# Kernel tuning notes

Hardware: AMD Instinct MI355X
Metric: run time of the kernel (lower is better)

The kernel has to match this reference:

```python
import jax, jax.numpy as jnp
import numpy as np

B, T, N, I = 64, 12, 307, 3   # batch, timesteps, nodes, input features
R, D = 64, 10                 # rnn_units, embed_dim


def setup_inputs() -> dict:
    key = jax.random.key(0)
    ks = iter(jax.random.split(key, 64))
    def p(*shape):
        return jax.random.normal(next(ks), shape, jnp.float32) * 0.1
    return dict(
        x=jax.random.normal(next(ks), (B, T, N, I), jnp.float32),
        node_emb1=p(N, D), node_emb2=p(N, D),
        # x_embedding MLP: 1 -> 16 -> 2 -> D
        xe_w1=p(16, 1), xe_b1=p(16), xe_w2=p(2, 16), xe_b2=p(2), xe_w3=p(D, 2), xe_b3=p(D),
        # fc1 MLP: I -> 16 -> 2 -> D
        fc1_w1=p(16, I), fc1_b1=p(16), fc1_w2=p(2, 16), fc1_b2=p(2), fc1_w3=p(D, 2), fc1_b3=p(D),
        # fc2 MLP: R -> 16 -> 2 -> D
        fc2_w1=p(16, R), fc2_b1=p(16), fc2_w2=p(2, 16), fc2_b2=p(2), fc2_w3=p(D, 2), fc2_b3=p(D),
        # GRU1 (input D -> hidden R), gates ordered r,z,n as in torch
        gru1_wih=p(3 * R, D), gru1_whh=p(3 * R, R), gru1_bih=p(3 * R), gru1_bhh=p(3 * R),
        # GRU2 (input R -> hidden R)
        gru2_wih=p(3 * R, R), gru2_whh=p(3 * R, R), gru2_bih=p(3 * R), gru2_bhh=p(3 * R),
        weights_pool=p(D, R, R), bias_pool=p(D, R),
        # 1x1 conv == linear over channels: [R, 2R]
        diff_w=p(R, 2 * R), diff_b=p(R),
    )


def _mlp(x, w1, b1, w2, b2, w3, b3):
    h = jax.nn.sigmoid(x @ w1.T + b1)
    h = jax.nn.sigmoid(h @ w2.T + b2)
    return h @ w3.T + b3


def _gru(xs, h0, wih, whh, bih, bhh):
    # xs: [T, B', Din]; torch GRU gate order: r, z, n
    xw = xs @ wih.T + bih  # precompute input projections [T, B', 3R]
    def step(h, xw_t):
        hw = h @ whh.T + bhh
        xr, xz, xn = jnp.split(xw_t, 3, -1)
        hr, hz, hn = jnp.split(hw, 3, -1)
        r = jax.nn.sigmoid(xr + hr)
        z = jax.nn.sigmoid(xz + hz)
        n = jnp.tanh(xn + r * hn)
        h = (1.0 - z) * n + z * h
        return h, h
    _, out = jax.lax.scan(step, h0, xw)
    return out  # [T, B', R]


def reference(x, node_emb1, node_emb2,
              xe_w1, xe_b1, xe_w2, xe_b2, xe_w3, xe_b3,
              fc1_w1, fc1_b1, fc1_w2, fc1_b2, fc1_w3, fc1_b3,
              fc2_w1, fc2_b1, fc2_w2, fc2_b2, fc2_w3, fc2_b3,
              gru1_wih, gru1_whh, gru1_bih, gru1_bhh,
              gru2_wih, gru2_whh, gru2_bih, gru2_bhh,
              weights_pool, bias_pool, diff_w, diff_b):
    # --- feature-level dynamic dependency ---
    node_embed = _mlp(x[..., None], xe_w1, xe_b1, xe_w2, xe_b2, xe_w3, xe_b3)  # [B,T,N,I,D]
    supports_node2 = jax.nn.relu(jnp.einsum('btnjd,btnid->btnji', node_embed, node_embed))  # [B,T,N,I,I]
    # x1 = eye(I) @ x == x (identity support kept implicit)
    x2 = jnp.einsum('btnji,btni->btnj', supports_node2, x)
    input_for_fc1 = x + x2
    g1_in = _mlp(input_for_fc1, fc1_w1, fc1_b1, fc1_w2, fc1_b2, fc1_w3, fc1_b3)  # [B,T,N,D]
    g1_in = jnp.transpose(g1_in, (1, 0, 2, 3)).reshape(T, B * N, D)
    h0 = jnp.zeros((B * N, R), jnp.float32)
    out1 = _gru(g1_in, h0, gru1_wih, gru1_whh, gru1_bih, gru1_bhh).reshape(T, B, N, R)
    # --- node-level dynamic dependency ---
    filt = _mlp(out1, fc2_w1, fc2_b1, fc2_w2, fc2_b2, fc2_w3, fc2_b3)  # [T,B,N,D]
    nodevec = jnp.tanh(node_emb1 * filt)  # broadcast [N,D] over [T,B,N,D]
    supports2 = jax.nn.relu(jnp.einsum('tbnd,tbmd->tbnm', nodevec, nodevec))  # [T,B,N,N]
    # x_g1 = eye(N) @ out1 == out1
    x_g = out1 + jnp.einsum('tbnm,tbmc->tbnc', supports2, out1)
    weights = jnp.einsum('nd,dcr->ncr', node_emb2, weights_pool)  # [N,R,R]
    bias = node_emb2 @ bias_pool                                   # [N,R]
    diff1 = jnp.einsum('tbnc,ncr->tbnr', x_g, weights) + bias      # [T,B,N,R]
    # --- 1x1 conv over channels + GRU2 (dropout in eval mode: identity) ---
    cat = jnp.concatenate([out1, diff1], axis=-1)                  # [T,B,N,2R]
    g2_in = jnp.einsum('tbnc,rc->tbnr', cat, diff_w) + diff_b      # [T,B,N,R]
    out2 = _gru(g2_in.reshape(T, B * N, R), h0, gru2_wih, gru2_whh, gru2_bih, gru2_bhh)
    return jnp.transpose(out2.reshape(T, B, N, R), (1, 0, 2, 3))   # [B,T,N,R]
```

## Files before the change

kernel.cpp:

```cpp
#include <hip/hip_runtime.h>
#include <hip/hip_fp16.h>
#include <math.h>

#define B_ 64
#define T_ 12
#define N_ 307
#define I_ 3
#define R_ 64
#define D_ 10
#define M_ (B_*N_)
#define TM_ (T_*M_)

typedef _Float16 f16x8 __attribute__((ext_vector_type(8)));
typedef float f32x4 __attribute__((ext_vector_type(4)));

__device__ __forceinline__ float sigm(float x){ return 1.f/(1.f+__expf(-x)); }

__device__ __forceinline__ unsigned pkh(float a, float b){
  unsigned r;
  asm("v_cvt_pkrtz_f16_f32 %0, %1, %2" : "=v"(r) : "v"(a), "v"(b));
  return r;
}

__global__ __launch_bounds__(256) void k_stageA(
    const float* __restrict__ x,
    const float* __restrict__ xw1, const float* __restrict__ xb1,
    const float* __restrict__ xw2, const float* __restrict__ xb2,
    const float* __restrict__ xw3, const float* __restrict__ xb3,
    const float* __restrict__ fw1, const float* __restrict__ fb1,
    const float* __restrict__ fw2, const float* __restrict__ fb2,
    const float* __restrict__ fw3, const float* __restrict__ fb3,
    float* __restrict__ g1)
{
  int idx = blockIdx.x*256 + threadIdx.x;
  int t = idx / M_;
  int m = idx - t*M_;
  int b = m / N_;
  int n = m - b*N_;
  const float* xp = x + (((size_t)b*T_ + t)*N_ + n)*I_;
  float xv[3] = {xp[0], xp[1], xp[2]};
  float e[3][10];
  #pragma unroll
  for (int i=0;i<3;++i){
    float h1[16];
    #pragma unroll
    for (int u=0;u<16;++u) h1[u] = sigm(xv[i]*xw1[u] + xb1[u]);
    float h2[2];
    #pragma unroll
    for (int v=0;v<2;++v){
      float a = xb2[v];
      #pragma unroll
      for (int u=0;u<16;++u) a += h1[u]*xw2[v*16+u];
      h2[v] = sigm(a);
    }
    #pragma unroll
    for (int d=0;d<10;++d) e[i][d] = xb3[d] + h2[0]*xw3[d*2] + h2[1]*xw3[d*2+1];
  }
  float in1[3];
  #pragma unroll
  for (int j=0;j<3;++j){
    float acc = 0.f;
    #pragma unroll
    for (int i=0;i<3;++i){
      float s = 0.f;
      #pragma unroll
      for (int d=0;d<10;++d) s += e[j][d]*e[i][d];
      s = fmaxf(s, 0.f);
      acc += s*xv[i];
    }
    in1[j] = xv[j] + acc;
  }
  float h1[16];
  #pragma unroll
  for (int u=0;u<16;++u)
    h1[u] = sigm(fb1[u] + in1[0]*fw1[u*3] + in1[1]*fw1[u*3+1] + in1[2]*fw1[u*3+2]);
  float h2[2];
  #pragma unroll
  for (int v=0;v<2;++v){
    float a = fb2[v];
    #pragma unroll
    for (int u=0;u<16;++u) a += h1[u]*fw2[v*16+u];
    h2[v] = sigm(a);
  }
  float* gp = g1 + (size_t)idx*10;
  #pragma unroll
  for (int d=0;d<10;++d) gp[d] = fb3[d] + h2[0]*fw3[d*2] + h2[1]*fw3[d*2+1];
}

__global__ __launch_bounds__(256) void k_wn(
    const float* __restrict__ emb2, const float* __restrict__ wpool,
    const float* __restrict__ bpool, float* __restrict__ Wn, float* __restrict__ bn)
{
  int n = blockIdx.x; int tid = threadIdx.x;
  __shared__ float e_s[10];
  if (tid < 10) e_s[tid] = emb2[n*10 + tid];
  __syncthreads();
  #pragma unroll
  for (int e=0;e<16;++e){
    int i = e*256 + tid;
    float a = 0.f;
    #pragma unroll
    for (int d=0;d<10;++d) a += e_s[d]*wpool[(size_t)d*4096 + i];
    Wn[(size_t)n*4096 + i] = a;
  }
  if (tid < 64){
    float a = 0.f;
    #pragma unroll
    for (int d=0;d<10;++d) a += e_s[d]*bpool[d*64 + tid];
    bn[n*64 + tid] = a;
  }
}

__global__ __launch_bounds__(256) void k_wf(
    const float* __restrict__ Wn, const float* __restrict__ bn,
    const float* __restrict__ dw, const float* __restrict__ db,
    float* __restrict__ Wf, float* __restrict__ bf)
{
  int n = blockIdx.x; int tid = threadIdx.x;
  __shared__ float WnS[64*68];
  __shared__ float dwBT[64*68];
  __shared__ float bn_s[64];
  for (int idx = tid; idx < 4096; idx += 256) {
    int c = idx >> 6, r = idx & 63;
    WnS[c*68 + r] = Wn[(size_t)n*4096 + idx];
  }
  for (int idx = tid; idx < 4096; idx += 256) {
    int u = idx >> 6, r = idx & 63;
    dwBT[r*68 + u] = dw[u*128 + 64 + r];
  }
  if (tid < 64) bn_s[tid] = bn[n*64 + tid];
  __syncthreads();
  int u = tid & 63, cg = tid >> 6;
  #pragma unroll
  for (int j = 0; j < 16; ++j) {
    int c = cg*16 + j;
    float acc = 0.f;
    #pragma unroll 8
    for (int r = 0; r < 64; ++r) acc += WnS[c*68 + r] * dwBT[r*68 + u];
    Wf[(size_t)n*4096 + u*64 + c] = acc;
  }
  if (tid < 64) {
    float acc = db[tid];
    #pragma unroll 8
    for (int r = 0; r < 64; ++r) acc += bn_s[r] * dwBT[r*68 + tid];
    bf[n*64 + tid] = acc;
  }
}

__global__ __launch_bounds__(256) void k_wpackM(
    const float* __restrict__ wih2, const float* __restrict__ whh2,
    const float* __restrict__ wih1, const float* __restrict__ whh1,
    unsigned* __restrict__ Wh2, unsigned* __restrict__ Wx2,
    unsigned* __restrict__ Wh1, unsigned* __restrict__ Wx1)
{
  int i = blockIdx.x*256 + threadIdx.x;
  if (i < 192*32) {
    int wr = i >> 5, p = i & 31;
    Wh2[i] = pkh(whh2[wr*64 + 2*p], whh2[wr*64 + 2*p + 1]);
    Wx2[i] = pkh(wih2[wr*64 + 2*p], wih2[wr*64 + 2*p + 1]);
    Wh1[i] = pkh(whh1[wr*64 + 2*p], whh1[wr*64 + 2*p + 1]);
  }
  int j = i - 192*32;
  if (j >= 0 && j < 192*16) {
    int wr = j >> 4, p = j & 15;
    Wx1[j] = (p < 5) ? pkh(wih1[wr*10 + 2*p], wih1[wr*10 + 2*p + 1]) : 0u;
  }
}

template<int DIN, bool WFIN>
__global__ __launch_bounds__(256, 3) void k_gruM(
    const float* __restrict__ xseq,
    const unsigned* __restrict__ Whf,
    const unsigned* __restrict__ Wxf,
    const float* __restrict__ bih, const float* __restrict__ bhh,
    float* __restrict__ o_out)
{
  constexpr int XPR = (DIN == 64) ? 32 : 16;
  constexpr int XKS = XPR / 16;
  constexpr int XST = XPR + 4;
  __shared__ __align__(16) unsigned Ah_s[16*36];
  __shared__ __align__(16) unsigned Ax_s[16*XST];
  const int tid = threadIdx.x;
  const int lane = tid & 63, w = tid >> 6;
  const int fr = lane & 15, fq = lane >> 4;
  const int row0 = blockIdx.x * 16;
  const int u = w*16 + fr;

  f16x8 bh_r[2], bh_z[2], bh_n[2];
  #pragma unroll
  for (int ks = 0; ks < 2; ++ks) {
    bh_r[ks] = *(const f16x8*)&Whf[(size_t)u*32        + ks*16 + fq*4];
    bh_z[ks] = *(const f16x8*)&Whf[(size_t)(64+u)*32   + ks*16 + fq*4];
    bh_n[ks] = *(const f16x8*)&Whf[(size_t)(128+u)*32  + ks*16 + fq*4];
  }
  f16x8 bx_r[XKS], bx_z[XKS], bx_n[XKS];
  #pragma unroll
  for (int ks = 0; ks < XKS; ++ks) {
    bx_r[ks] = *(const f16x8*)&Wxf[(size_t)u*XPR       + ks*16 + fq*4];
    bx_z[ks] = *(const f16x8*)&Wxf[(size_t)(64+u)*XPR  + ks*16 + fq*4];
    bx_n[ks] = *(const f16x8*)&Wxf[(size_t)(128+u)*XPR + ks*16 + fq*4];
  }

  const float brc = bih[u]     + bhh[u];
  const float bzc = bih[64+u]  + bhh[64+u];
  const float bxn = bih[128+u];
  const float bhn = bhh[128+u];

  for (int i = tid; i < 16*36;  i += 256) Ah_s[i] = 0u;
  for (int i = tid; i < 16*XST; i += 256) Ax_s[i] = 0u;
  __syncthreads();

  size_t obase[4];
  #pragma unroll
  for (int reg = 0; reg < 4; ++reg) {
    int g = row0 + fq*4 + reg;
    if (WFIN) { int bb = g / N_, nn = g - bb*N_; obase[reg] = (((size_t)bb*T_)*N_ + nn)*64 + u; }
    else      { obase[reg] = (size_t)g*64 + u; }
  }
  const size_t tstep = WFIN ? (size_t)N_*64 : (size_t)M_*64;
  float hreg[4] = {0.f, 0.f, 0.f, 0.f};

  for (int t = 0; t < T_; ++t) {
    if (DIN == 64) {
      #pragma unroll
      for (int it = 0; it < 2; ++it) {
        int idx = tid + it*256;
        int row = idx >> 5, p = idx & 31;
        const float2 v = *(const float2*)&xseq[((size_t)t*M_ + row0 + row)*64 + 2*p];
        Ax_s[row*XST + p] = pkh(v.x, v.y);
      }
    } else {
      if (tid < 80) {
        int row = tid / 5, p = tid - (tid/5)*5;
        const float2 v = *(const float2*)&xseq[((size_t)t*M_ + row0 + row)*10 + 2*p];
        Ax_s[row*XST + p] = pkh(v.x, v.y);
      }
    }
    __syncthreads();

    f32x4 ar  = {0.f,0.f,0.f,0.f}, az  = {0.f,0.f,0.f,0.f};
    f32x4 anh = {0.f,0.f,0.f,0.f}, anx = {0.f,0.f,0.f,0.f};
    #pragma unroll
    for (int ks = 0; ks < 2; ++ks) {
      f16x8 ah = *(const f16x8*)&Ah_s[fr*36 + ks*16 + fq*4];
      ar  = __builtin_amdgcn_mfma_f32_16x16x32_f16(ah, bh_r[ks], ar,  0,0,0);
      az  = __builtin_amdgcn_mfma_f32_16x16x32_f16(ah, bh_z[ks], az,  0,0,0);
      anh = __builtin_amdgcn_mfma_f32_16x16x32_f16(ah, bh_n[ks], anh, 0,0,0);
    }
    #pragma unroll
    for (int ks = 0; ks < XKS; ++ks) {
      f16x8 ax = *(const f16x8*)&Ax_s[fr*XST + ks*16 + fq*4];
      ar  = __builtin_amdgcn_mfma_f32_16x16x32_f16(ax, bx_r[ks], ar,  0,0,0);
      az  = __builtin_amdgcn_mfma_f32_16x16x32_f16(ax, bx_z[ks], az,  0,0,0);
      anx = __builtin_amdgcn_mfma_f32_16x16x32_f16(ax, bx_n[ks], anx, 0,0,0);
    }

    float o_new[4];
    #pragma unroll
    for (int reg = 0; reg < 4; ++reg) {
      float rg = sigm(ar[reg] + brc);
      float zg = sigm(az[reg] + bzc);
      float ng = tanhf(anx[reg] + bxn + rg*(anh[reg] + bhn));
      o_new[reg] = (1.f - zg)*ng + zg*hreg[reg];
      hreg[reg] = o_new[reg];
    }
    #pragma unroll
    for (int reg = 0; reg < 4; ++reg)
      o_out[obase[reg] + (size_t)t*tstep] = o_new[reg];

    unsigned pk[4];
    #pragma unroll
    for (int reg = 0; reg < 4; ++reg) {
      float pr = __shfl_xor(o_new[reg], 1);
      pk[reg] = pkh(o_new[reg], pr);
    }
    __syncthreads();
    if ((fr & 1) == 0) {
      #pragma unroll
      for (int reg = 0; reg < 4; ++reg)
        Ah_s[(fq*4 + reg)*36 + w*8 + (fr >> 1)] = pk[reg];
    }
  }
}

__global__ __launch_bounds__(256) void k_stageC(
    const float* __restrict__ out1, const float* __restrict__ emb1,
    const float* __restrict__ w1, const float* __restrict__ b1,
    const float* __restrict__ w2, const float* __restrict__ b2,
    const float* __restrict__ w3, const float* __restrict__ b3,
    float* __restrict__ ndv)
{
  int idx = blockIdx.x*256 + threadIdx.x;
  int m = idx % M_;
  int n = m % N_;
  float rv[64];
  const float4* r4 = (const float4*)(out1 + (size_t)idx*64);
  #pragma unroll
  for (int q=0;q<16;++q){ float4 v=r4[q]; rv[q*4]=v.x; rv[q*4+1]=v.y; rv[q*4+2]=v.z; rv[q*4+3]=v.w; }
  float h1[16];
  for (int u=0;u<16;++u){
    float a = b1[u];
    const float* wr = w1 + u*64;
    #pragma unroll
    for (int c=0;c<64;++c) a += rv[c]*wr[c];
    h1[u] = sigm(a);
  }
  float h2[2];
  #pragma unroll
  for (int v=0;v<2;++v){
    float a = b2[v];
    #pragma unroll
    for (int u=0;u<16;++u) a += h1[u]*w2[v*16+u];
    h2[v] = sigm(a);
  }
  #pragma unroll
  for (int d=0;d<10;++d){
    float f = b3[d] + h2[0]*w3[d*2] + h2[1]*w3[d*2+1];
    ndv[(size_t)idx*10 + d] = tanhf(emb1[n*10+d]*f);
  }
}

__global__ __launch_bounds__(256, 3) void k_stageDM(
    const float* __restrict__ ndv, const float* __restrict__ out1, float* __restrict__ xg)
{
  const int tb = blockIdx.x;
  const int tid = threadIdx.x;
  const int lane = tid & 63, wid = tid >> 6;
  const int fr = lane & 15, fq = lane >> 4;

  __shared__ __align__(16) unsigned Vp_s[320*20];
  __shared__ __align__(16) unsigned P_s[64*36];
  __shared__ __align__(16) unsigned O_s[2][64*36];

  for (int i = tid; i < 320*20; i += 256) {
    int nn = i / 20, p = i - (i/20)*20;
    float a = 0.f, b = 0.f;
    if (nn < N_ && p < 5) {
      const float2 v = *(const float2*)&ndv[((size_t)tb*N_ + nn)*10 + 2*p];
      a = v.x; b = v.y;
    }
    Vp_s[i] = pkh(a, b);
  }

  const float* ob = out1 + (size_t)tb*N_*64;

  for (int it = tid; it < 512; it += 256) {
    int p = it & 31, cg = it >> 5;
    int m0 = 2*p;
    float4 a = make_float4(0.f,0.f,0.f,0.f), b = a;
    if (m0     < N_) a = *(const float4*)&ob[(size_t)m0*64 + cg*4];
    if (m0 + 1 < N_) b = *(const float4*)&ob[(size_t)(m0+1)*64 + cg*4];
    int c0 = cg*4;
    O_s[0][(c0+0)*36 + p] = pkh(a.x, b.x);
    O_s[0][(c0+1)*36 + p] = pkh(a.y, b.y);
    O_s[0][(c0+2)*36 + p] = pkh(a.z, b.z);
    O_s[0][(c0+3)*36 + p] = pkh(a.w, b.w);
  }
  __syncthreads();

  f32x4 acc[5][4];
  #pragma unroll
  for (int a = 0; a < 5; ++a)
    #pragma unroll
    for (int c = 0; c < 4; ++c)
      acc[a][c] = (f32x4){0.f, 0.f, 0.f, 0.f};

  for (int k = 0; k < 5; ++k) {
    const int cur = k & 1;
    const int mc = k*64;
    if (k < 4) {
      int mcn = mc + 64;
      for (int it = tid; it < 512; it += 256) {
        int p = it & 31, cg = it >> 5;
        int m0 = mcn + 2*p;
        float4 a = make_float4(0.f,0.f,0.f,0.f), b = a;
        if (m0     < N_) a = *(const float4*)&ob[(size_t)m0*64 + cg*4];
        if (m0 + 1 < N_) b = *(const float4*)&ob[(size_t)(m0+1)*64 + cg*4];
        int c0 = cg*4;
        O_s[cur^1][(c0+0)*36 + p] = pkh(a.x, b.x);
        O_s[cur^1][(c0+1)*36 + p] = pkh(a.y, b.y);
        O_s[cur^1][(c0+2)*36 + p] = pkh(a.z, b.z);
        O_s[cur^1][(c0+3)*36 + p] = pkh(a.w, b.w);
      }
    }
    f16x8 va[4];
    #pragma unroll
    for (int mt = 0; mt < 4; ++mt)
      va[mt] = *(const f16x8*)&Vp_s[(mc + mt*16 + fr)*20 + fq*4];
    f16x8 bo[2][4];
    #pragma unroll
    for (int ks = 0; ks < 2; ++ks)
      #pragma unroll
      for (int ct = 0; ct < 4; ++ct)
        bo[ks][ct] = *(const f16x8*)&O_s[cur][(ct*16 + fr)*36 + ks*16 + fq*4];

    #pragma unroll
    for (int j = 0; j < 5; ++j) {
      int nt = wid + 4*j;
      f16x8 vb = *(const f16x8*)&Vp_s[(nt*16 + fr)*20 + fq*4];
      #pragma unroll
      for (int mt = 0; mt < 4; ++mt) {
        f32x4 s = (f32x4){0.f,0.f,0.f,0.f};
        s = __builtin_amdgcn_mfma_f32_16x16x32_f16(va[mt], vb, s, 0, 0, 0);
        unsigned p0 = pkh(fmaxf(s[0],0.f), fmaxf(s[1],0.f));
        unsigned p1 = pkh(fmaxf(s[2],0.f), fmaxf(s[3],0.f));
        *(uint2*)&P_s[(wid*16 + fr)*36 + mt*8 + fq*2] = make_uint2(p0, p1);
      }
      #pragma unroll
      for (int ks = 0; ks < 2; ++ks) {
        f16x8 af = *(const f16x8*)&P_s[(wid*16 + fr)*36 + ks*16 + fq*4];
        #pragma unroll
        for (int ct = 0; ct < 4; ++ct)
          acc[j][ct] = __builtin_amdgcn_mfma_f32_16x16x32_f16(af, bo[ks][ct], acc[j][ct], 0, 0, 0);
      }
    }
    __syncthreads();
  }

  #pragma unroll
  for (int j = 0; j < 5; ++j) {
    #pragma unroll
    for (int ct = 0; ct < 4; ++ct) {
      int col = ct*16 + fr;
      #pragma unroll
      for (int reg = 0; reg < 4; ++reg) {
        int n = (wid + 4*j)*16 + fq*4 + reg;
        if (n < N_) {
          size_t base = (size_t)tb*N_*64 + (size_t)n*64 + col;
          xg[base] = out1[base] + acc[j][ct][reg];
        }
      }
    }
  }
}

__global__ __launch_bounds__(256) void k_stageEM(
    const float* xg_in, const float* __restrict__ out1,
    const float* __restrict__ Wf, const float* __restrict__ dw,
    const float* __restrict__ bf,
    float* xg_out)
{
  int n = blockIdx.y;
  int tile = blockIdx.x;
  const int tid = threadIdx.x;
  const int lane = tid & 63, w = tid >> 6;
  const int fr = lane & 15, fq = lane >> 4;
  __shared__ __align__(16) unsigned As[64*68];
  __shared__ __align__(16) unsigned Bs[64*68];
  __shared__ float bf_s[64];

  for (int idx = tid; idx < 1024; idx += 256) {
    int row = idx >> 4, c4 = idx & 15;
    size_t g = ((size_t)(tile*64 + row)*N_ + n)*64 + c4*4;
    float4 o  = *(const float4*)&out1[g];
    float4 xv = *(const float4*)&xg_in[g];
    As[row*68 + c4*2]          = pkh(o.x, o.y);
    As[row*68 + c4*2 + 1]      = pkh(o.z, o.w);
    As[row*68 + 32 + c4*2]     = pkh(xv.x, xv.y);
    As[row*68 + 32 + c4*2 + 1] = pkh(xv.z, xv.w);
    int u = row;
    float4 da = *(const float4*)&dw[u*128 + c4*4];
    float4 wf = *(const float4*)&Wf[(size_t)n*4096 + u*64 + c4*4];
    Bs[u*68 + c4*2]          = pkh(da.x, da.y);
    Bs[u*68 + c4*2 + 1]      = pkh(da.z, da.w);
    Bs[u*68 + 32 + c4*2]     = pkh(wf.x, wf.y);
    Bs[u*68 + 32 + c4*2 + 1] = pkh(wf.z, wf.w);
  }
  if (tid < 64) bf_s[tid] = bf[n*64 + tid];
  __syncthreads();

  f32x4 acc[4];
  #pragma unroll
  for (int ct = 0; ct < 4; ++ct) acc[ct] = (f32x4){0.f,0.f,0.f,0.f};

  #pragma unroll
  for (int ks = 0; ks < 4; ++ks) {
    f16x8 af = *(const f16x8*)&As[(w*16 + fr)*68 + ks*16 + fq*4];
    #pragma unroll
    for (int ct = 0; ct < 4; ++ct) {
      f16x8 bfr = *(const f16x8*)&Bs[(ct*16 + fr)*68 + ks*16 + fq*4];
      acc[ct] = __builtin_amdgcn_mfma_f32_16x16x32_f16(af, bfr, acc[ct], 0, 0, 0);
    }
  }

  #pragma unroll
  for (int ct = 0; ct < 4; ++ct) {
    int u = ct*16 + fr;
    float bfv = bf_s[u];
    #pragma unroll
    for (int reg = 0; reg < 4; ++reg) {
      int row = w*16 + fq*4 + reg;
      xg_out[((size_t)(tile*64 + row)*N_ + n)*64 + u] = acc[ct][reg] + bfv;
    }
  }
}

extern "C" void kernel_launch(void* const* d_in, const int* in_sizes, int n_in,
                              void* d_out, int out_size, void* d_ws, size_t ws_size,
                              hipStream_t stream)
{
  (void)in_sizes; (void)n_in; (void)out_size;
  const float* x    = (const float*)d_in[0];
  const float* emb1 = (const float*)d_in[1];
  const float* emb2 = (const float*)d_in[2];
  const float* xw1  = (const float*)d_in[3];
  const float* xb1  = (const float*)d_in[4];
  const float* xw2  = (const float*)d_in[5];
  const float* xb2  = (const float*)d_in[6];
  const float* xw3  = (const float*)d_in[7];
  const float* xb3  = (const float*)d_in[8];
  const float* fw1  = (const float*)d_in[9];
  const float* fb1  = (const float*)d_in[10];
  const float* fw2  = (const float*)d_in[11];
  const float* fb2  = (const float*)d_in[12];
  const float* fw3  = (const float*)d_in[13];
  const float* fb3  = (const float*)d_in[14];
  const float* c2w1 = (const float*)d_in[15];
  const float* c2b1 = (const float*)d_in[16];
  const float* c2w2 = (const float*)d_in[17];
  const float* c2b2 = (const float*)d_in[18];
  const float* c2w3 = (const float*)d_in[19];
  const float* c2b3 = (const float*)d_in[20];
  const float* g1wih= (const float*)d_in[21];
  const float* g1whh= (const float*)d_in[22];
  const float* g1bih= (const float*)d_in[23];
  const float* g1bhh= (const float*)d_in[24];
  const float* g2wih= (const float*)d_in[25];
  const float* g2whh= (const float*)d_in[26];
  const float* g2bih= (const float*)d_in[27];
  const float* g2bhh= (const float*)d_in[28];
  const float* wpool= (const float*)d_in[29];
  const float* bpool= (const float*)d_in[30];
  const float* dww  = (const float*)d_in[31];
  const float* dwb  = (const float*)d_in[32];
  float* out = (float*)d_out;

  float* ws = (float*)d_ws;
  float* g1_in = ws;
  float* out1  = g1_in + (size_t)TM_*10;
  float* ndv   = out1 + (size_t)TM_*64;
  float* xg    = ndv + (size_t)TM_*10;
  float* Wn    = xg + (size_t)TM_*64;
  float* bn    = Wn + (size_t)N_*4096;
  float* Wf    = bn + (size_t)N_*64;
  float* bf    = Wf + (size_t)N_*4096;
  unsigned* Wh2f = (unsigned*)(bf + (size_t)N_*64);
  unsigned* Wx2f = Wh2f + 192*32;
  unsigned* Wh1f = Wx2f + 192*32;
  unsigned* Wx1f = Wh1f + 192*32;
  size_t need = ((size_t)((char*)(Wx1f + 192*16) - (char*)ws));
  if (ws_size < need) return;

  k_stageA<<<TM_/256, 256, 0, stream>>>(x, xw1,xb1,xw2,xb2,xw3,xb3, fw1,fb1,fw2,fb2,fw3,fb3, g1_in);
  k_wn<<<N_, 256, 0, stream>>>(emb2, wpool, bpool, Wn, bn);
  k_wf<<<N_, 256, 0, stream>>>(Wn, bn, dww, dwb, Wf, bf);
  k_wpackM<<<(192*32 + 192*16 + 255)/256, 256, 0, stream>>>(
      g2wih, g2whh, g1wih, g1whh, Wh2f, Wx2f, Wh1f, Wx1f);

  k_gruM<10,false><<<M_/16, 256, 0, stream>>>(g1_in, Wh1f, Wx1f, g1bih, g1bhh, out1);

  k_stageC<<<TM_/256, 256, 0, stream>>>(out1, emb1, c2w1,c2b1,c2w2,c2b2,c2w3,c2b3, ndv);
  k_stageDM<<<T_*B_, 256, 0, stream>>>(ndv, out1, xg);
  k_stageEM<<<dim3(12, N_), 256, 0, stream>>>(xg, out1, Wf, dww, bf, xg);

  k_gruM<64,true><<<M_/16, 256, 0, stream>>>(xg, Wh2f, Wx2f, g2bih, g2bhh, out);
}
```

Before: 227.5 us.

## Fuse fc2 MLP into graph-conv kernel and reassociate per-node weight precompute

The fc2 MLP plus tanh node-vector computation, previously a separate kernel writing ndv to global memory, now runs inside k_stageDM on the out1 rows the block already owns, and the result is packed directly into shared memory. The weight precompute is reassociated so the 1x1-conv matrix is applied once per embedding dimension (10 blocks) rather than per node (307 blocks), and a cheap per-node combine follows. This removes one launch, the ndv round trip, and most of the per-node 64x64 matmuls. The cost is that only threads 0-63 of each block do a second MLP row, so the MLP work runs on few threads per block, and registers rise in an occupancy-constrained kernel.

```diff
diff --git a/kernel.cpp b/kernel.cpp
--- a/kernel.cpp
+++ b/kernel.cpp
@@ -87,9 +87,46 @@
   for (int d=0;d<10;++d) gp[d] = fb3[d] + h2[0]*fw3[d*2] + h2[1]*fw3[d*2+1];
 }
 
-__global__ __launch_bounds__(256) void k_wn(
-    const float* __restrict__ emb2, const float* __restrict__ wpool,
-    const float* __restrict__ bpool, float* __restrict__ Wn, float* __restrict__ bn)
+__global__ __launch_bounds__(256) void k_prep(
+    const float* __restrict__ wpool, const float* __restrict__ bpool,
+    const float* __restrict__ dw,
+    float* __restrict__ Wp2, float* __restrict__ bp2)
+{
+  int d = blockIdx.x; int tid = threadIdx.x;
+  __shared__ float WpS[64*68];
+  __shared__ float dwBT[64*68];
+  __shared__ float bp_s[64];
+  for (int idx = tid; idx < 4096; idx += 256) {
+    int c = idx >> 6, r = idx & 63;
+    WpS[c*68 + r] = wpool[(size_t)d*4096 + idx];
+  }
+  for (int idx = tid; idx < 4096; idx += 256) {
+    int u = idx >> 6, r = idx & 63;
+    dwBT[r*68 + u] = dw[u*128 + 64 + r];
+  }
+  if (tid < 64) bp_s[tid] = bpool[d*64 + tid];
+  __syncthreads();
+  int u = tid & 63, cg = tid >> 6;
+  #pragma unroll
+  for (int j = 0; j < 16; ++j) {
+    int c = cg*16 + j;
+    float acc = 0.f;
+    #pragma unroll 8
+    for (int r = 0; r < 64; ++r) acc += WpS[c*68 + r] * dwBT[r*68 + u];
+    Wp2[(size_t)d*4096 + u*64 + c] = acc;
+  }
+  if (tid < 64) {
+    float acc = 0.f;
+    #pragma unroll 8
+    for (int r = 0; r < 64; ++r) acc += bp_s[r] * dwBT[r*68 + tid];
+    bp2[d*64 + tid] = acc;
+  }
+}
+
+__global__ __launch_bounds__(256) void k_wnf(
+    const float* __restrict__ emb2, const float* __restrict__ Wp2,
+    const float* __restrict__ bp2, const float* __restrict__ db,
+    float* __restrict__ Wf, float* __restrict__ bf)
 {
   int n = blockIdx.x; int tid = threadIdx.x;
   __shared__ float e_s[10];
@@ -100,50 +137,14 @@
     int i = e*256 + tid;
     float a = 0.f;
     #pragma unroll
-    for (int d=0;d<10;++d) a += e_s[d]*wpool[(size_t)d*4096 + i];
-    Wn[(size_t)n*4096 + i] = a;
+    for (int d=0;d<10;++d) a += e_s[d]*Wp2[(size_t)d*4096 + i];
+    Wf[(size_t)n*4096 + i] = a;
   }
   if (tid < 64){
-    float a = 0.f;
-    #pragma unroll
-    for (int d=0;d<10;++d) a += e_s[d]*bpool[d*64 + tid];
-    bn[n*64 + tid] = a;
-  }
-}
-
-__global__ __launch_bounds__(256) void k_wf(
-    const float* __restrict__ Wn, const float* __restrict__ bn,
-    const float* __restrict__ dw, const float* __restrict__ db,
-    float* __restrict__ Wf, float* __restrict__ bf)
-{
-  int n = blockIdx.x; int tid = threadIdx.x;
-  __shared__ float WnS[64*68];
-  __shared__ float dwBT[64*68];
-  __shared__ float bn_s[64];
-  for (int idx = tid; idx < 4096; idx += 256) {
-    int c = idx >> 6, r = idx & 63;
-    WnS[c*68 + r] = Wn[(size_t)n*4096 + idx];
-  }
-  for (int idx = tid; idx < 4096; idx += 256) {
-    int u = idx >> 6, r = idx & 63;
-    dwBT[r*68 + u] = dw[u*128 + 64 + r];
-  }
-  if (tid < 64) bn_s[tid] = bn[n*64 + tid];
-  __syncthreads();
-  int u = tid & 63, cg = tid >> 6;
-  #pragma unroll
-  for (int j = 0; j < 16; ++j) {
-    int c = cg*16 + j;
-    float acc = 0.f;
-    #pragma unroll 8
-    for (int r = 0; r < 64; ++r) acc += WnS[c*68 + r] * dwBT[r*68 + u];
-    Wf[(size_t)n*4096 + u*64 + c] = acc;
-  }
-  if (tid < 64) {
-    float acc = db[tid];
-    #pragma unroll 8
-    for (int r = 0; r < 64; ++r) acc += bn_s[r] * dwBT[r*68 + tid];
-    bf[n*64 + tid] = acc;
+    float a = db[tid];
+    #pragma unroll
+    for (int d=0;d<10;++d) a += e_s[d]*bp2[d*64 + tid];
+    bf[n*64 + tid] = a;
   }
 }
 
@@ -283,45 +284,12 @@
   }
 }
 
-__global__ __launch_bounds__(256) void k_stageC(
+__global__ __launch_bounds__(256, 3) void k_stageDM(
     const float* __restrict__ out1, const float* __restrict__ emb1,
     const float* __restrict__ w1, const float* __restrict__ b1,
     const float* __restrict__ w2, const float* __restrict__ b2,
     const float* __restrict__ w3, const float* __restrict__ b3,
-    float* __restrict__ ndv)
-{
-  int idx = blockIdx.x*256 + threadIdx.x;
-  int m = idx % M_;
-  int n = m % N_;
-  float rv[64];
-  const float4* r4 = (const float4*)(out1 + (size_t)idx*64);
-  #pragma unroll
-  for (int q=0;q<16;++q){ float4 v=r4[q]; rv[q*4]=v.x; rv[q*4+1]=v.y; rv[q*4+2]=v.z; rv[q*4+3]=v.w; }
-  float h1[16];
-  for (int u=0;u<16;++u){
-    float a = b1[u];
-    const float* wr = w1 + u*64;
-    #pragma unroll
-    for (int c=0;c<64;++c) a += rv[c]*wr[c];
-    h1[u] = sigm(a);
-  }
-  float h2[2];
-  #pragma unroll
-  for (int v=0;v<2;++v){
-    float a = b2[v];
-    #pragma unroll
-    for (int u=0;u<16;++u) a += h1[u]*w2[v*16+u];
-    h2[v] = sigm(a);
-  }
-  #pragma unroll
-  for (int d=0;d<10;++d){
-    float f = b3[d] + h2[0]*w3[d*2] + h2[1]*w3[d*2+1];
-    ndv[(size_t)idx*10 + d] = tanhf(emb1[n*10+d]*f);
-  }
-}
-
-__global__ __launch_bounds__(256, 3) void k_stageDM(
-    const float* __restrict__ ndv, const float* __restrict__ out1, float* __restrict__ xg)
+    float* __restrict__ xg)
 {
   const int tb = blockIdx.x;
   const int tid = threadIdx.x;
@@ -332,17 +300,45 @@
   __shared__ __align__(16) unsigned P_s[64*36];
   __shared__ __align__(16) unsigned O_s[2][64*36];
 
-  for (int i = tid; i < 320*20; i += 256) {
-    int nn = i / 20, p = i - (i/20)*20;
-    float a = 0.f, b = 0.f;
-    if (nn < N_ && p < 5) {
-      const float2 v = *(const float2*)&ndv[((size_t)tb*N_ + nn)*10 + 2*p];
-      a = v.x; b = v.y;
-    }
-    Vp_s[i] = pkh(a, b);
-  }
-
   const float* ob = out1 + (size_t)tb*N_*64;
+
+  for (int rr = tid; rr < 320; rr += 256) {
+    float nd[10];
+    if (rr < N_) {
+      float rv[64];
+      const float4* r4 = (const float4*)(ob + (size_t)rr*64);
+      #pragma unroll
+      for (int q=0;q<16;++q){ float4 v=r4[q]; rv[q*4]=v.x; rv[q*4+1]=v.y; rv[q*4+2]=v.z; rv[q*4+3]=v.w; }
+      float h1v[16];
+      for (int u=0;u<16;++u){
+        float a = b1[u];
+        const float* wr = w1 + u*64;
+        #pragma unroll
+        for (int c=0;c<64;++c) a += rv[c]*wr[c];
+        h1v[u] = sigm(a);
+      }
+      float h2v[2];
+      #pragma unroll
+      for (int v=0;v<2;++v){
+        float a = b2[v];
+        #pragma unroll
+        for (int u=0;u<16;++u) a += h1v[u]*w2[v*16+u];
+        h2v[v] = sigm(a);
+      }
+      #pragma unroll
+      for (int d=0;d<10;++d){
+        float f = b3[d] + h2v[0]*w3[d*2] + h2v[1]*w3[d*2+1];
+        nd[d] = tanhf(emb1[rr*10+d]*f);
+      }
+    } else {
+      #pragma unroll
+      for (int d=0;d<10;++d) nd[d] = 0.f;
+    }
+    #pragma unroll
+    for (int p=0;p<5;++p) Vp_s[rr*20 + p] = pkh(nd[2*p], nd[2*p+1]);
+    #pragma unroll
+    for (int p=5;p<20;++p) Vp_s[rr*20 + p] = 0u;
+  }
 
   for (int it = tid; it < 512; it += 256) {
     int p = it & 31, cg = it >> 5;
@@ -538,13 +534,12 @@
   float* ws = (float*)d_ws;
   float* g1_in = ws;
   float* out1  = g1_in + (size_t)TM_*10;
-  float* ndv   = out1 + (size_t)TM_*64;
-  float* xg    = ndv + (size_t)TM_*10;
-  float* Wn    = xg + (size_t)TM_*64;
-  float* bn    = Wn + (size_t)N_*4096;
-  float* Wf    = bn + (size_t)N_*64;
+  float* xg    = out1 + (size_t)TM_*64;
+  float* Wf    = xg + (size_t)TM_*64;
   float* bf    = Wf + (size_t)N_*4096;
-  unsigned* Wh2f = (unsigned*)(bf + (size_t)N_*64);
+  float* Wp2   = bf + (size_t)N_*64;
+  float* bp2   = Wp2 + 10*4096;
+  unsigned* Wh2f = (unsigned*)(bp2 + 10*64);
   unsigned* Wx2f = Wh2f + 192*32;
   unsigned* Wh1f = Wx2f + 192*32;
   unsigned* Wx1f = Wh1f + 192*32;
@@ -552,15 +547,14 @@
   if (ws_size < need) return;
 
   k_stageA<<<TM_/256, 256, 0, stream>>>(x, xw1,xb1,xw2,xb2,xw3,xb3, fw1,fb1,fw2,fb2,fw3,fb3, g1_in);
-  k_wn<<<N_, 256, 0, stream>>>(emb2, wpool, bpool, Wn, bn);
-  k_wf<<<N_, 256, 0, stream>>>(Wn, bn, dww, dwb, Wf, bf);
+  k_prep<<<10, 256, 0, stream>>>(wpool, bpool, dww, Wp2, bp2);
+  k_wnf<<<N_, 256, 0, stream>>>(emb2, Wp2, bp2, dwb, Wf, bf);
   k_wpackM<<<(192*32 + 192*16 + 255)/256, 256, 0, stream>>>(
       g2wih, g2whh, g1wih, g1whh, Wh2f, Wx2f, Wh1f, Wx1f);
 
   k_gruM<10,false><<<M_/16, 256, 0, stream>>>(g1_in, Wh1f, Wx1f, g1bih, g1bhh, out1);
 
-  k_stageC<<<TM_/256, 256, 0, stream>>>(out1, emb1, c2w1,c2b1,c2w2,c2b2,c2w3,c2b3, ndv);
-  k_stageDM<<<T_*B_, 256, 0, stream>>>(ndv, out1, xg);
+  k_stageDM<<<T_*B_, 256, 0, stream>>>(out1, emb1, c2w1,c2b1,c2w2,c2b2,c2w3,c2b3, xg);
   k_stageEM<<<dim3(12, N_), 256, 0, stream>>>(xg, out1, Wf, dww, bf, xg);
 
   k_gruM<64,true><<<M_/16, 256, 0, stream>>>(xg, Wh2f, Wx2f, g2bih, g2bhh, out);
```

After: 226.3 us. Within noise of the previous version (-0.5%).
